# Kernel optimization log

Hardware: AMD Instinct MI355X
Metric: run time of the kernel (lower is better)

Reference implementation:

```python
import jax, jax.numpy as jnp
import numpy as np

VOCAB, EMB, HID, NTAG, SEQ = 50000, 256, 512, 20, 8192
H = HID // 2  # per-direction hidden size


def _lstm_dir(x, Wih, Whh, bih, bhh, reverse):
    # x: [S, E]; PyTorch gate order i, f, g, o
    h0 = jnp.zeros((H,), x.dtype)
    c0 = jnp.zeros((H,), x.dtype)
    b = bih + bhh
    xg = x @ Wih.T + b  # [S, 4H] precompute input projection

    def step(carry, xt):
        h, c = carry
        gates = xt + h @ Whh.T
        i, f, g, o = jnp.split(gates, 4)
        i = jax.nn.sigmoid(i)
        f = jax.nn.sigmoid(f)
        g = jnp.tanh(g)
        o = jax.nn.sigmoid(o)
        c = f * c + i * g
        h = o * jnp.tanh(c)
        return (h, c), h

    _, hs = jax.lax.scan(step, (h0, c0), xg, reverse=reverse)
    return hs  # [S, H]


def _viterbi(emissions, start_trans, end_trans, trans):
    # emissions [S, T]; torchcrf-style Viterbi decode
    score0 = start_trans + emissions[0]

    def fwd(score, em):
        tot = score[:, None] + trans          # [T_from, T_to]
        bp = jnp.argmax(tot, axis=0)          # best previous tag per next tag
        score = jnp.max(tot, axis=0) + em
        return score, bp

    final, bps = jax.lax.scan(fwd, score0, emissions[1:])
    final = final + end_trans
    last = jnp.argmax(final).astype(jnp.int32)

    def back(tag, bp):
        prev = bp[tag].astype(jnp.int32)
        return prev, prev

    _, prevs = jax.lax.scan(back, last, bps, reverse=True)
    return jnp.concatenate([prevs, last[None]])  # [S]


def setup_inputs() -> dict:
    key = jax.random.key(0)
    ks = jax.random.split(key, 16)
    s = 0.1
    inp = {
        "sentence": jax.random.randint(ks[0], (SEQ,), 0, VOCAB, dtype=jnp.int64)
                    if jax.config.read("jax_enable_x64") else
                    jax.random.randint(ks[0], (SEQ,), 0, VOCAB, dtype=jnp.int32),
        "embed": jax.random.normal(ks[1], (VOCAB, EMB), jnp.float32),
        "Wih_f": jax.random.normal(ks[2], (4 * H, EMB), jnp.float32) * s,
        "Whh_f": jax.random.normal(ks[3], (4 * H, H), jnp.float32) * s,
        "bih_f": jax.random.normal(ks[4], (4 * H,), jnp.float32) * s,
        "bhh_f": jax.random.normal(ks[5], (4 * H,), jnp.float32) * s,
        "Wih_b": jax.random.normal(ks[6], (4 * H, EMB), jnp.float32) * s,
        "Whh_b": jax.random.normal(ks[7], (4 * H, H), jnp.float32) * s,
        "bih_b": jax.random.normal(ks[8], (4 * H,), jnp.float32) * s,
        "bhh_b": jax.random.normal(ks[9], (4 * H,), jnp.float32) * s,
        "Wout": jax.random.normal(ks[10], (NTAG, HID), jnp.float32) * s,
        "bout": jax.random.normal(ks[11], (NTAG,), jnp.float32) * s,
        "start_trans": jax.random.normal(ks[12], (NTAG,), jnp.float32) * s,
        "end_trans": jax.random.normal(ks[13], (NTAG,), jnp.float32) * s,
        "trans": jax.random.normal(ks[14], (NTAG, NTAG), jnp.float32) * s,
    }
    return inp


def reference(sentence, embed, Wih_f, Whh_f, bih_f, bhh_f,
              Wih_b, Whh_b, bih_b, bhh_b, Wout, bout,
              start_trans, end_trans, trans):
    x = embed[sentence]                                  # [S, E]
    h_f = _lstm_dir(x, Wih_f, Whh_f, bih_f, bhh_f, reverse=False)
    h_b = _lstm_dir(x, Wih_b, Whh_b, bih_b, bhh_b, reverse=True)
    lstm_out = jnp.concatenate([h_f, h_b], axis=-1)      # [S, HID]; dropout is eval-mode identity
    emissions = lstm_out @ Wout.T + bout                 # [S, T]
    path = _viterbi(emissions, start_trans, end_trans, trans)
    return path
```

## Files before the change

kernel.cpp:

```cpp
#include <hip/hip_runtime.h>
#include <hip/hip_bf16.h>


#define S    8192
#define E    256
#define Hh   256
#define G    1024
#define NT   20
#define NB   4
#define NCHUNK 128
#define CLEN   64
#define SENT 0x7FC0DEADu

__global__ __launch_bounds__(256) void sentinel_fill(unsigned int* __restrict__ lo_u)
{
    size_t base = (size_t)blockIdx.x * 1024 + threadIdx.x;
    #pragma unroll
    for (int i = 0; i < 4; ++i)
        __hip_atomic_store(&lo_u[base + (size_t)i * 256], SENT,
                           __ATOMIC_RELAXED, __HIP_MEMORY_SCOPE_AGENT);
}

__global__ __launch_bounds__(1024, 4) void xg_project(
    const int* __restrict__ sent, const float* __restrict__ embed,
    const float* __restrict__ Wih_f, const float* __restrict__ bih_f, const float* __restrict__ bhh_f,
    const float* __restrict__ Wih_b, const float* __restrict__ bih_b, const float* __restrict__ bhh_b,
    float* __restrict__ xg)
{
    const int tb  = blockIdx.x;
    const int rb  = blockIdx.y;
    const int dir = blockIdx.z;
    const int tid = threadIdx.x;
    const int q   = tid >> 8;
    const int idx = tid & 255;
    const int r   = rb * 256 + idx;
    const float* Wih = dir ? Wih_b : Wih_f;

    __shared__ __align__(16) float4 xs4[32 * 64];
    __shared__ float psum[1024];

    const int t0 = tb * 32;
    #pragma unroll
    for (int i = 0; i < 2; ++i) {
        int qq  = i * 1024 + tid;
        int row = qq >> 6;
        int c4  = qq & 63;
        int widx = sent[t0 + row];
        xs4[qq] = *(const float4*)(embed + (size_t)widx * E + (size_t)c4 * 4);
    }

    float w[64];
    #pragma unroll
    for (int k = 0; k < 64; k += 4) {
        float4 v = *(const float4*)(Wih + (size_t)r * E + q * 64 + k);
        w[k] = v.x; w[k+1] = v.y; w[k+2] = v.z; w[k+3] = v.w;
    }
    float bias = 0.f;
    if (tid < 256) bias = dir ? (bih_b[r] + bhh_b[r]) : (bih_f[r] + bhh_f[r]);
    __syncthreads();

    const float* xs = (const float*)xs4 + q * 64;
    float* outb = xg + ((size_t)dir * S + t0) * G + r;
    for (int tt = 0; tt < 32; ++tt) {
        float a0 = 0.f, a1 = 0.f, a2 = 0.f, a3 = 0.f;
        #pragma unroll
        for (int k = 0; k < 64; k += 4) {
            float4 h4 = *(const float4*)(xs + tt * E + k);
            a0 = fmaf(w[k],   h4.x, a0);
            a1 = fmaf(w[k+1], h4.y, a1);
            a2 = fmaf(w[k+2], h4.z, a2);
            a3 = fmaf(w[k+3], h4.w, a3);
        }
        psum[tid] = (a0 + a1) + (a2 + a3);
        __syncthreads();
        if (tid < 256)
            outb[(size_t)tt * G] = bias +
                ((psum[idx] + psum[idx + 256]) + (psum[idx + 512] + psum[idx + 768]));
        __syncthreads();
    }
}

__global__ __launch_bounds__(1024, 4) void lstm_scan_mc(
    const float* __restrict__ xg,
    const float* __restrict__ Whh_f,
    const float* __restrict__ Whh_b,
    float* __restrict__ out)
{
    const int b    = blockIdx.x;
    const int dir  = blockIdx.y;
    const int tid  = threadIdx.x;
    const int q    = tid >> 8;
    const int idx  = tid & 255;
    const int gate = idx >> 6;
    const int hloc = idx & 63;
    const int hidx = b * 64 + hloc;
    const int row  = gate * Hh + hidx;
    const float* W   = dir ? Whh_b : Whh_f;
    const float* xgd = xg + (size_t)dir * S * G;

    float w[64];
    #pragma unroll
    for (int k = 0; k < 64; k += 4) {
        float4 v = *(const float4*)(W + (size_t)row * Hh + q * 64 + k);
        w[k] = v.x; w[k+1] = v.y; w[k+2] = v.z; w[k+3] = v.w;
    }

    __shared__ __align__(16) float h_lds[Hh];
    __shared__ float psum[1024];
    __shared__ float gates_lds[256];
    if (tid < Hh) h_lds[tid] = 0.f;
    float c = 0.f;

    const int t0 = dir ? (S - 1) : 0;
    const int dt = dir ? -1 : 1;
    float xg_cur = (tid < 256) ? xgd[(size_t)t0 * G + row] : 0.f;
    __syncthreads();

    for (int s = 0; s < S; ++s) {
        const int t = t0 + dt * s;
        float xg_next = 0.f;
        if (tid < 256 && s + 1 < S) xg_next = xgd[(size_t)(t + dt) * G + row];

        const float* hh = (const float*)h_lds + q * 64;
        float a0 = 0.f, a1 = 0.f, a2 = 0.f, a3 = 0.f;
        #pragma unroll
        for (int k = 0; k < 64; k += 4) {
            float4 h4 = *(const float4*)(hh + k);
            a0 = fmaf(w[k],   h4.x, a0);
            a1 = fmaf(w[k+1], h4.y, a1);
            a2 = fmaf(w[k+2], h4.z, a2);
            a3 = fmaf(w[k+3], h4.w, a3);
        }
        psum[tid] = (a0 + a1) + (a2 + a3);
        __syncthreads();

        if (tid < 256) {
            float acc = xg_cur +
                ((psum[idx] + psum[idx + 256]) + (psum[idx + 512] + psum[idx + 768]));
            float a = (gate == 2) ? tanhf(acc) : 1.f / (1.f + expf(-acc));
            gates_lds[idx] = a;
        }
        __syncthreads();

        if (tid < 64) {
            float iv = gates_lds[hloc];
            float fv = gates_lds[64 + hloc];
            float gv = gates_lds[128 + hloc];
            float ov = gates_lds[192 + hloc];
            c = fv * c + iv * gv;
            float h = ov * tanhf(c);
            __hip_atomic_store(out + (size_t)t * 512 + dir * Hh + hidx, h,
                               __ATOMIC_RELAXED, __HIP_MEMORY_SCOPE_AGENT);
            h_lds[hidx] = h;
        }
        if (s + 1 < S && tid < Hh && (tid >> 6) != b) {
            const unsigned int* srcp =
                (const unsigned int*)(out + (size_t)t * 512 + dir * Hh + tid);
            unsigned int v;
            do {
                v = __hip_atomic_load(srcp, __ATOMIC_RELAXED,
                                      __HIP_MEMORY_SCOPE_AGENT);
            } while (v == SENT);
            h_lds[tid] = __uint_as_float(v);
        }
        __syncthreads();
        xg_cur = xg_next;
    }
}

__global__ __launch_bounds__(256) void emissions_kernel(
    const float* __restrict__ lo,
    const float* __restrict__ Wout,
    const float* __restrict__ bout,
    float* __restrict__ em)
{
    int gid = blockIdx.x * blockDim.x + threadIdx.x;
    if (gid >= S * NT) return;
    int t = gid / NT;
    int j = gid - t * NT;
    const float* x = lo + (size_t)t * 512;
    const float* w = Wout + (size_t)j * 512;
    float a0 = 0.f, a1 = 0.f, a2 = 0.f, a3 = 0.f;
    #pragma unroll 8
    for (int k = 0; k < 512; k += 4) {
        float4 xv = *(const float4*)(x + k);
        float4 wv = *(const float4*)(w + k);
        a0 = fmaf(xv.x, wv.x, a0);
        a1 = fmaf(xv.y, wv.y, a1);
        a2 = fmaf(xv.z, wv.z, a2);
        a3 = fmaf(xv.w, wv.w, a3);
    }
    em[gid] = bout[j] + ((a0 + a1) + (a2 + a3));
}

__device__ __forceinline__ void vit_cmb(float& va, int& ia, float vb, int ib) {
    if (vb > va) { va = vb; ia = ib; }
}

__global__ __launch_bounds__(64) void viterbi_fwd(
    const float* __restrict__ em,
    const float* __restrict__ start_trans,
    const float* __restrict__ end_trans,
    const float* __restrict__ trans,
    unsigned char* __restrict__ bp,
    int* __restrict__ last_out)
{
    const int lane = threadIdx.x;
    const bool act = (lane < NT);
    const int j = act ? lane : 0;

    __shared__ __align__(16) float sc[24];

    float tc[NT];
    #pragma unroll
    for (int i = 0; i < NT; ++i) tc[i] = trans[i * NT + j];

    float snew = start_trans[j] + em[j];
    if (act) bp[lane] = (unsigned char)lane;
    float e0 = em[NT + j];
    float e1 = em[2 * NT + j];

    for (int t = 1; t < S; ++t) {
        if (act) sc[lane] = snew;
        __builtin_amdgcn_wave_barrier();
        float s0[NT];
        #pragma unroll
        for (int i = 0; i < NT; i += 4) {
            float4 v = *(const float4*)(sc + i);
            s0[i] = v.x; s0[i+1] = v.y; s0[i+2] = v.z; s0[i+3] = v.w;
        }
        __builtin_amdgcn_wave_barrier();

        float e2 = (t + 2 < S) ? em[(size_t)(t + 2) * NT + j] : 0.f;

        float cv[NT];
        #pragma unroll
        for (int i = 0; i < NT; ++i) cv[i] = s0[i] + tc[i];

        float v1[10]; int i1[10];
        #pragma unroll
        for (int u = 0; u < 10; ++u) {
            v1[u] = cv[2*u]; i1[u] = 2*u;
            vit_cmb(v1[u], i1[u], cv[2*u+1], 2*u+1);
        }
        float v2[5]; int i2[5];
        #pragma unroll
        for (int u = 0; u < 5; ++u) {
            v2[u] = v1[2*u]; i2[u] = i1[2*u];
            vit_cmb(v2[u], i2[u], v1[2*u+1], i1[2*u+1]);
        }
        float v3a = v2[0]; int i3a = i2[0];
        vit_cmb(v3a, i3a, v2[1], i2[1]);
        float v3b = v2[2]; int i3b = i2[2];
        vit_cmb(v3b, i3b, v2[3], i2[3]);
        vit_cmb(v3a, i3a, v3b, i3b);
        vit_cmb(v3a, i3a, v2[4], i2[4]);

        snew = v3a + e0;
        if (act) bp[(size_t)t * NT + lane] = (unsigned char)i3a;
        e0 = e1; e1 = e2;
    }

    if (act) sc[lane] = snew + end_trans[j];
    __builtin_amdgcn_wave_barrier();
    {
        float s0[NT];
        #pragma unroll
        for (int i = 0; i < NT; i += 4) {
            float4 v = *(const float4*)(sc + i);
            s0[i] = v.x; s0[i+1] = v.y; s0[i+2] = v.z; s0[i+3] = v.w;
        }
        float bv = s0[0]; int bi = 0;
        #pragma unroll
        for (int i = 1; i < NT; ++i) vit_cmb(bv, bi, s0[i], i);
        if (lane == 0) *last_out = bi;
    }
}

__global__ __launch_bounds__(64) void bt_maps(
    const unsigned char* __restrict__ bp, unsigned char* __restrict__ maps)
{
    __shared__ unsigned char lbp[CLEN * NT];
    const int c = blockIdx.x, tid = threadIdx.x;
    const unsigned* src = (const unsigned*)(bp + (size_t)c * CLEN * NT);
    unsigned* dst = (unsigned*)lbp;
    for (int q = tid; q < CLEN * NT / 4; q += 64) dst[q] = src[q];
    __syncthreads();
    if (tid < NT) {
        int x = tid;
        for (int t = CLEN - 1; t >= 0; --t) x = lbp[t * NT + x];
        maps[c * NT + tid] = (unsigned char)x;
    }
}

__global__ __launch_bounds__(64) void bt_boundary(
    const unsigned char* __restrict__ maps, const int* __restrict__ last_out,
    int* __restrict__ btags)
{
    __shared__ unsigned char m[NCHUNK * NT];
    const int tid = threadIdx.x;
    for (int q = tid; q < NCHUNK * NT; q += 64) m[q] = maps[q];
    __syncthreads();
    if (tid == 0) {
        int x = *last_out;
        btags[NCHUNK - 1] = x;
        for (int c = NCHUNK - 1; c >= 1; --c) {
            x = m[c * NT + x];
            btags[c - 1] = x;
        }
    }
}

__global__ __launch_bounds__(64) void bt_emit(
    const unsigned char* __restrict__ bp, const int* __restrict__ btags,
    int* __restrict__ path)
{
    __shared__ unsigned char lbp[CLEN * NT];
    const int c = blockIdx.x, tid = threadIdx.x;
    const unsigned* src = (const unsigned*)(bp + (size_t)c * CLEN * NT);
    unsigned* dst = (unsigned*)lbp;
    for (int q = tid; q < CLEN * NT / 4; q += 64) dst[q] = src[q];
    __syncthreads();
    if (tid == 0) {
        int x = btags[c];
        path[c * CLEN + CLEN - 1] = x;
        for (int t = CLEN - 1; t >= 1; --t) {
            x = lbp[t * NT + x];
            path[c * CLEN + t - 1] = x;
        }
    }
}

extern "C" void kernel_launch(void* const* d_in, const int* in_sizes, int n_in,
                              void* d_out, int out_size, void* d_ws, size_t ws_size,
                              hipStream_t stream) {
    const int*   sent   = (const int*)  d_in[0];
    const float* embed  = (const float*)d_in[1];
    const float* Wih_f  = (const float*)d_in[2];
    const float* Whh_f  = (const float*)d_in[3];
    const float* bih_f  = (const float*)d_in[4];
    const float* bhh_f  = (const float*)d_in[5];
    const float* Wih_b  = (const float*)d_in[6];
    const float* Whh_b  = (const float*)d_in[7];
    const float* bih_b  = (const float*)d_in[8];
    const float* bhh_b  = (const float*)d_in[9];
    const float* Wout   = (const float*)d_in[10];
    const float* bout   = (const float*)d_in[11];
    const float* start_trans = (const float*)d_in[12];
    const float* end_trans   = (const float*)d_in[13];
    const float* trans       = (const float*)d_in[14];
    int* path = (int*)d_out;

    char* ws = (char*)d_ws;
    size_t off = 0;
    float* xg = (float*)(ws + off); off += (size_t)2 * S * G * 4;
    float* lo = (float*)(ws + off); off += (size_t)S * 512 * 4;
    float* em = (float*)(ws + off); off += (size_t)S * NT * 4;
    unsigned char* bp   = (unsigned char*)(ws + off); off += (size_t)S * NT;
    unsigned char* maps = (unsigned char*)(ws + off); off += 4096;
    int* btags = (int*)(ws + off); off += 1024;
    int* lastp = (int*)(ws + off); off += 256;

    sentinel_fill<<<dim3(4096), 256, 0, stream>>>((unsigned int*)lo);
    xg_project<<<dim3(S / 32, 4, 2), 1024, 0, stream>>>(
        sent, embed, Wih_f, bih_f, bhh_f, Wih_b, bih_b, bhh_b, xg);
    lstm_scan_mc<<<dim3(NB, 2), 1024, 0, stream>>>(xg, Whh_f, Whh_b, lo);
    emissions_kernel<<<dim3((S * NT + 255) / 256), 256, 0, stream>>>(lo, Wout, bout, em);
    viterbi_fwd<<<dim3(1), 64, 0, stream>>>(em, start_trans, end_trans, trans, bp, lastp);
    bt_maps<<<dim3(NCHUNK), 64, 0, stream>>>(bp, maps);
    bt_boundary<<<dim3(1), 64, 0, stream>>>(maps, lastp, btags);
    bt_emit<<<dim3(NCHUNK), 64, 0, stream>>>(bp, btags, path);
}
```

Measured before the change: 16.27 ms.

## Interleave gates per hidden unit, shuffle-combine cell update, split polling warps

The gate index now runs fastest within each group of four threads, so the four gate activations for a hidden unit sit in adjacent lanes. The cell update uses wavefront shuffles instead of a shared-memory gate buffer, which removes one block-wide barrier per timestep. Polling of other blocks' hidden state moves off the gate-computing threads onto dedicated wavefronts, plus a second 'echo' set that sleeps briefly and then polls the same words again. This shortens the serial critical path per step, at the cost of redundant global polling traffic and duplicate LDS writes.

Result: slower. 17.18 ms (+5.6%).

```diff
diff --git a/kernel.cpp b/kernel.cpp
--- a/kernel.cpp
+++ b/kernel.cpp
@@ -80,7 +80,7 @@
     }
 }
 
-__global__ __launch_bounds__(1024, 4) void lstm_scan_mc(
+__global__ __launch_bounds__(1024, 4) void lstm_scan_gi(
     const float* __restrict__ xg,
     const float* __restrict__ Whh_f,
     const float* __restrict__ Whh_b,
@@ -91,8 +91,8 @@
     const int tid  = threadIdx.x;
     const int q    = tid >> 8;
     const int idx  = tid & 255;
-    const int gate = idx >> 6;
-    const int hloc = idx & 63;
+    const int gate = idx & 3;
+    const int hloc = idx >> 2;
     const int hidx = b * 64 + hloc;
     const int row  = gate * Hh + hidx;
     const float* W   = dir ? Whh_b : Whh_f;
@@ -107,9 +107,15 @@
 
     __shared__ __align__(16) float h_lds[Hh];
     __shared__ float psum[1024];
-    __shared__ float gates_lds[256];
     if (tid < Hh) h_lds[tid] = 0.f;
     float c = 0.f;
+
+    const bool isPoll = (tid >= 256 && tid < 448);
+    const bool isEcho = (tid >= 448 && tid < 640);
+    const int  pl     = isPoll ? (tid - 256) : (isEcho ? (tid - 448) : 0);
+    const int  pi     = pl >> 6;
+    const int  word   = pl & 63;
+    const int  pb     = pi + (pi >= b);
 
     const int t0 = dir ? (S - 1) : 0;
     const int dt = dir ? -1 : 1;
@@ -138,30 +144,35 @@
             float acc = xg_cur +
                 ((psum[idx] + psum[idx + 256]) + (psum[idx + 512] + psum[idx + 768]));
             float a = (gate == 2) ? tanhf(acc) : 1.f / (1.f + expf(-acc));
-            gates_lds[idx] = a;
-        }
-        __syncthreads();
-
-        if (tid < 64) {
-            float iv = gates_lds[hloc];
-            float fv = gates_lds[64 + hloc];
-            float gv = gates_lds[128 + hloc];
-            float ov = gates_lds[192 + hloc];
-            c = fv * c + iv * gv;
-            float h = ov * tanhf(c);
-            __hip_atomic_store(out + (size_t)t * 512 + dir * Hh + hidx, h,
-                               __ATOMIC_RELAXED, __HIP_MEMORY_SCOPE_AGENT);
-            h_lds[hidx] = h;
-        }
-        if (s + 1 < S && tid < Hh && (tid >> 6) != b) {
+            float fv = __shfl_down(a, 1);
+            float gv = __shfl_down(a, 2);
+            float ov = __shfl_down(a, 3);
+            if (gate == 0) {
+                c = fv * c + a * gv;
+                float h = ov * tanhf(c);
+                __hip_atomic_store(out + (size_t)t * 512 + dir * Hh + hidx, h,
+                                   __ATOMIC_RELAXED, __HIP_MEMORY_SCOPE_AGENT);
+                h_lds[hidx] = h;
+            }
+        } else if (isPoll && s + 1 < S) {
             const unsigned int* srcp =
-                (const unsigned int*)(out + (size_t)t * 512 + dir * Hh + tid);
+                (const unsigned int*)(out + (size_t)t * 512 + dir * Hh + pb * 64 + word);
             unsigned int v;
             do {
                 v = __hip_atomic_load(srcp, __ATOMIC_RELAXED,
                                       __HIP_MEMORY_SCOPE_AGENT);
             } while (v == SENT);
-            h_lds[tid] = __uint_as_float(v);
+            h_lds[pb * 64 + word] = __uint_as_float(v);
+        } else if (isEcho && s + 1 < S) {
+            __builtin_amdgcn_s_sleep(4);
+            const unsigned int* srcp =
+                (const unsigned int*)(out + (size_t)t * 512 + dir * Hh + pb * 64 + word);
+            unsigned int v;
+            do {
+                v = __hip_atomic_load(srcp, __ATOMIC_RELAXED,
+                                      __HIP_MEMORY_SCOPE_AGENT);
+            } while (v == SENT);
+            h_lds[pb * 64 + word] = __uint_as_float(v);
         }
         __syncthreads();
         xg_cur = xg_next;
@@ -364,7 +375,7 @@
     sentinel_fill<<<dim3(4096), 256, 0, stream>>>((unsigned int*)lo);
     xg_project<<<dim3(S / 32, 4, 2), 1024, 0, stream>>>(
         sent, embed, Wih_f, bih_f, bhh_f, Wih_b, bih_b, bhh_b, xg);
-    lstm_scan_mc<<<dim3(NB, 2), 1024, 0, stream>>>(xg, Whh_f, Whh_b, lo);
+    lstm_scan_gi<<<dim3(NB, 2), 1024, 0, stream>>>(xg, Whh_f, Whh_b, lo);
     emissions_kernel<<<dim3((S * NT + 255) / 256), 256, 0, stream>>>(lo, Wout, bout, em);
     viterbi_fwd<<<dim3(1), 64, 0, stream>>>(em, start_trans, end_trans, trans, bp, lastp);
     bt_maps<<<dim3(NCHUNK), 64, 0, stream>>>(bp, maps);
```
